# Optimization experiments

Hardware: AMD Instinct MI355X
Metric: run time of the kernel (lower is better)

The kernel has to match this reference:

```python
import jax, jax.numpy as jnp
import numpy as np

N_CELL, N_TISSUE, H, NH = 200000, 2000, 256, 8
HD = H // NH
SCALE = HD ** -0.5
EPS = 1e-5


def _layernorm(x, g, b):
    m = jnp.mean(x, axis=-1, keepdims=True)
    v = jnp.mean((x - m) ** 2, axis=-1, keepdims=True)
    return (x - m) / jnp.sqrt(v + EPS) * g + b


def setup_inputs() -> dict:
    key = jax.random.key(0)
    ks = jax.random.split(key, 12)
    s = 0.02

    def lin(k):
        k1, k2 = jax.random.split(k)
        return (jax.random.normal(k1, (H, H), jnp.float32) * s,
                jax.random.normal(k2, (H,), jnp.float32) * s)

    Wq_bu, bq_bu = lin(ks[0])
    Wk_bu, bk_bu = lin(ks[1])
    Wv_bu, bv_bu = lin(ks[2])
    Wo_bu, bo_bu = lin(ks[3])
    Wv_td, bv_td = lin(ks[4])
    Wo_td, bo_td = lin(ks[5])
    return dict(
        cell_features=jax.random.normal(ks[6], (N_CELL, H), jnp.float32),
        tissue_features=jax.random.normal(ks[7], (N_TISSUE, H), jnp.float32),
        cluster_labels=jax.random.randint(ks[8], (N_CELL,), 0, N_TISSUE, dtype=jnp.int32),
        tissue_batch=jnp.zeros((N_TISSUE,), jnp.int32),
        Wq_bu=Wq_bu, bq_bu=bq_bu, Wk_bu=Wk_bu, bk_bu=bk_bu,
        Wv_bu=Wv_bu, bv_bu=bv_bu, Wo_bu=Wo_bu, bo_bu=bo_bu,
        Wv_td=Wv_td, bv_td=bv_td, Wo_td=Wo_td, bo_td=bo_td,
        ln_cell_g=jnp.ones((H,), jnp.float32), ln_cell_b=jnp.zeros((H,), jnp.float32),
        ln_tissue_g=jnp.ones((H,), jnp.float32), ln_tissue_b=jnp.zeros((H,), jnp.float32),
    )


def reference(cell_features, tissue_features, cluster_labels, tissue_batch,
              Wq_bu, bq_bu, Wk_bu, bk_bu, Wv_bu, bv_bu, Wo_bu, bo_bu,
              Wv_td, bv_td, Wo_td, bo_td,
              ln_cell_g, ln_cell_b, ln_tissue_g, ln_tissue_b):
    Nc = cell_features.shape[0]
    Nt = tissue_features.shape[0]

    # ---- bottom-up: each tissue node (1 query) attends over its cells (segment attention) ----
    Q = (tissue_features @ Wq_bu + bq_bu).reshape(Nt, NH, HD)   # [Nt, h, d]
    K = (cell_features @ Wk_bu + bk_bu).reshape(Nc, NH, HD)     # [Nc, h, d]
    V = (cell_features @ Wv_bu + bv_bu).reshape(Nc, NH, HD)     # [Nc, h, d]

    # per-cell score against its own cluster's tissue query
    scores = jnp.einsum('nhd,nhd->nh', K, Q[cluster_labels]) * SCALE  # [Nc, h]
    smax = jax.lax.stop_gradient(
        jax.ops.segment_max(scores, cluster_labels, num_segments=Nt))  # [Nt, h]
    ex = jnp.exp(scores - smax[cluster_labels])
    denom = jax.ops.segment_sum(ex, cluster_labels, num_segments=Nt)   # [Nt, h]
    w = ex / denom[cluster_labels]                                     # [Nc, h]
    attended = jax.ops.segment_sum(w[..., None] * V, cluster_labels,
                                   num_segments=Nt)                    # [Nt, h, d]
    attended = attended.reshape(Nt, H) @ Wo_bu + bo_bu

    counts = jax.ops.segment_sum(jnp.ones((Nc,), cell_features.dtype),
                                 cluster_labels, num_segments=Nt)
    tissue_updated = jnp.where(counts[:, None] > 0, attended, tissue_features)

    # ---- top-down: each cell attends to its single tissue token ----
    # softmax over a single key is identically 1, so q/k projections cancel:
    # attended_cell = out_proj(v_proj(tissue_updated[cluster]))
    td_per_tissue = (tissue_updated @ Wv_td + bv_td) @ Wo_td + bo_td   # [Nt, H]
    cell_updated = td_per_tissue[cluster_labels]                       # [Nc, H]

    cell_out = _layernorm(cell_features + cell_updated, ln_cell_g, ln_cell_b)
    tissue_out = _layernorm(tissue_features + tissue_updated, ln_tissue_g, ln_tissue_b)
    return (cell_out, tissue_out)
```

## Files before the change

### kernel.cpp

```cpp
#include <hip/hip_runtime.h>
#include <math.h>

#define NC 200000
#define NT 2000
#define HH 256
#define NH_ 8
#define SCALE 0.17677669529663687f
#define EPS 1e-5f
#define SLICE 128
#define PSLICES (NT + NC / SLICE + 1)
#define PSTRIDE 2056


__global__ void k_hist(const int* __restrict__ labels, int* __restrict__ counts) {
  int i = blockIdx.x * 256 + threadIdx.x;
  if (i < NC) atomicAdd(&counts[labels[i]], 1);
}

__global__ void k_scan(const int* __restrict__ counts, int* __restrict__ offsets,
                       int* __restrict__ soff) {
  int tid = threadIdx.x;
  int base = tid * 32;
  int la[32], lb[32];
  int sa = 0, sb = 0;
  #pragma unroll
  for (int k = 0; k < 32; k++) {
    int idx = base + k;
    int v = (idx < NT) ? counts[idx] : 0;
    la[k] = sa; lb[k] = sb;
    sa += v; sb += (v + SLICE - 1) / SLICE;
  }
  int ia_ = sa, ib_ = sb;
  #pragma unroll
  for (int d = 1; d < 64; d <<= 1) {
    int oa = __shfl_up(ia_, d, 64);
    int ob = __shfl_up(ib_, d, 64);
    if (tid >= d) { ia_ += oa; ib_ += ob; }
  }
  int ea = ia_ - sa, eb = ib_ - sb;
  #pragma unroll
  for (int k = 0; k < 32; k++) {
    int idx = base + k;
    if (idx < NT) { offsets[idx] = ea + la[k]; soff[idx] = eb + lb[k]; }
  }
  if (tid == 63) { offsets[NT] = ia_; soff[NT] = ib_; }
}

__global__ void k_slicemap(const int* __restrict__ soff, int* __restrict__ slice_t) {
  int t = blockIdx.x * 256 + threadIdx.x;
  if (t < NT) {
    int s0 = soff[t], s1 = soff[t + 1];
    for (int s = s0; s < s1; s++) slice_t[s] = t;
  }
}

__global__ void k_scatter(const int* __restrict__ labels, const int* __restrict__ offsets,
                          int* __restrict__ cursor, int* __restrict__ cindex) {
  int i = blockIdx.x * 256 + threadIdx.x;
  if (i < NC) {
    int c = labels[i];
    int pos = offsets[c] + atomicAdd(&cursor[c], 1);
    cindex[pos] = i;
  }
}


__global__ __launch_bounds__(256) void k_gemm_bias(
    const float* __restrict__ A, const float* __restrict__ W,
    const float* __restrict__ bias, float* __restrict__ C, int M)
{
  __shared__ float Al[16][33];
  __shared__ float Wl[32][HH];
  int tid = threadIdx.x;
  int r0 = blockIdx.x * 16;
  float acc[16];
  #pragma unroll
  for (int r = 0; r < 16; r++) acc[r] = 0.f;
  for (int k0 = 0; k0 < HH; k0 += 32) {
    for (int e = tid; e < 16 * 32; e += 256) {
      int r = e >> 5, k = e & 31;
      int row = r0 + r;
      Al[r][k] = (row < M) ? A[(size_t)row * HH + k0 + k] : 0.f;
    }
    for (int e = tid; e < 32 * HH; e += 256) {
      int k = e >> 8, j = e & 255;
      Wl[k][j] = W[(size_t)(k0 + k) * HH + j];
    }
    __syncthreads();
    for (int k = 0; k < 32; k++) {
      float w = Wl[k][tid];
      #pragma unroll
      for (int r = 0; r < 16; r++) acc[r] += Al[r][k] * w;
    }
    __syncthreads();
  }
  float bj = bias[tid];
  #pragma unroll
  for (int r = 0; r < 16; r++) {
    int row = r0 + r;
    if (row < M) C[(size_t)row * HH + tid] = acc[r] + bj;
  }
}


__global__ __launch_bounds__(256) void k_qproj(
    const float* __restrict__ Q, const float* __restrict__ Wk, float* __restrict__ Qproj)
{
  __shared__ float Al[64][33];
  __shared__ float Bl[32][257];
  int h = blockIdx.x & 7, tb = blockIdx.x >> 3;
  int t0 = tb * 64;
  int tid = threadIdx.x;
  for (int e = tid; e < 64 * 32; e += 256) {
    int r = e >> 5, d = e & 31;
    int t = t0 + r;
    Al[r][d] = (t < NT) ? Q[(size_t)t * HH + h * 32 + d] * SCALE : 0.f;
  }
  for (int e = tid; e < 256 * 32; e += 256) {
    int j = e >> 5, d = e & 31;
    Bl[d][j] = Wk[(size_t)j * HH + h * 32 + d];
  }
  __syncthreads();
  float acc[64];
  #pragma unroll
  for (int r = 0; r < 64; r++) acc[r] = 0.f;
  for (int d = 0; d < 32; d++) {
    float b = Bl[d][tid];
    #pragma unroll
    for (int r = 0; r < 64; r++) acc[r] += Al[r][d] * b;
  }
  for (int r = 0; r < 64; r++) {
    int t = t0 + r;
    if (t < NT) Qproj[((size_t)t * NH_ + h) * HH + tid] = acc[r];
  }
}

__global__ void k_bkq(const float* __restrict__ Q, const float* __restrict__ bk,
                      float* __restrict__ bkq) {
  int g = blockIdx.x * 256 + threadIdx.x;
  if (g < NT * NH_) {
    int t = g >> 3, h = g & 7;
    float s = 0.f;
    #pragma unroll
    for (int d = 0; d < 32; d++) s += bk[h * 32 + d] * Q[(size_t)t * HH + h * 32 + d];
    bkq[g] = s * SCALE;
  }
}


__global__ __launch_bounds__(256) void k_cellslice(
    const float* __restrict__ cell, const int* __restrict__ cindex,
    const int* __restrict__ offsets, const int* __restrict__ soff,
    const int* __restrict__ slice_t,
    const float* __restrict__ Qproj, const float* __restrict__ bkq,
    float* __restrict__ Pbuf)
{
  __shared__ float qp[NH_][HH];
  __shared__ float e_lds[SLICE][NH_];
  __shared__ float cwlds[NH_][HH];
  __shared__ float red[4][NH_];

  int s = blockIdx.x;
  if (s >= soff[NT]) return;
  int t = slice_t[s];
  int l = s - soff[t];
  int c0 = offsets[t] + l * SLICE;
  int c1 = min(c0 + SLICE, offsets[t + 1]);
  int nc = c1 - c0;

  int tid = threadIdx.x;
  int w = tid >> 6, lane = tid & 63, slot = lane >> 3, g = lane & 7;

  for (int e = tid; e < NH_ * HH / 4; e += 256)
    ((float4*)qp)[e] = ((const float4*)(Qproj + (size_t)t * NH_ * HH))[e];
  float bq[NH_];
  #pragma unroll
  for (int h = 0; h < NH_; h++) bq[h] = bkq[t * NH_ + h];
  __syncthreads();

  int nsweep = (nc + 15) >> 4;
  for (int j = w; j < nsweep; j += 4) {
    int bb = c0 + j * 16;
    int ia = bb + slot, ib = bb + 8 + slot;
    int na = cindex[min(ia, c1 - 1)];
    int nb = cindex[min(ib, c1 - 1)];
    float4 xa[8], xb[8];
    #pragma unroll
    for (int k = 0; k < 8; k++)
      xa[k] = *reinterpret_cast<const float4*>(&cell[(size_t)na * HH + g * 4 + 32 * k]);
    #pragma unroll
    for (int k = 0; k < 8; k++)
      xb[k] = *reinterpret_cast<const float4*>(&cell[(size_t)nb * HH + g * 4 + 32 * k]);

    float pa[NH_], pb[NH_];
    #pragma unroll
    for (int h = 0; h < NH_; h++) { pa[h] = 0.f; pb[h] = 0.f; }
    #pragma unroll
    for (int h = 0; h < NH_; h++) {
      #pragma unroll
      for (int k = 0; k < 8; k++) {
        float4 q = *reinterpret_cast<const float4*>(&qp[h][g * 4 + 32 * k]);
        pa[h] += xa[k].x * q.x + xa[k].y * q.y + xa[k].z * q.z + xa[k].w * q.w;
        pb[h] += xb[k].x * q.x + xb[k].y * q.y + xb[k].z * q.z + xb[k].w * q.w;
      }
    }
    #pragma unroll
    for (int d = 1; d < 8; d <<= 1) {
      #pragma unroll
      for (int h = 0; h < NH_; h++) {
        pa[h] += __shfl_xor(pa[h], d, 64);
        pb[h] += __shfl_xor(pb[h], d, 64);
      }
    }
    float ea[NH_], eb[NH_];
    #pragma unroll
    for (int h = 0; h < NH_; h++) {
      ea[h] = __expf(pa[h] + bq[h]);
      eb[h] = __expf(pb[h] + bq[h]);
    }
    if (g == 0) {
      if (ia < c1) {
        *reinterpret_cast<float4*>(&e_lds[ia - c0][0]) = make_float4(ea[0], ea[1], ea[2], ea[3]);
        *reinterpret_cast<float4*>(&e_lds[ia - c0][4]) = make_float4(ea[4], ea[5], ea[6], ea[7]);
      }
      if (ib < c1) {
        *reinterpret_cast<float4*>(&e_lds[ib - c0][0]) = make_float4(eb[0], eb[1], eb[2], eb[3]);
        *reinterpret_cast<float4*>(&e_lds[ib - c0][4]) = make_float4(eb[4], eb[5], eb[6], eb[7]);
      }
    }
  }
  __syncthreads();

  float cw[NH_][4];
  float dsum[NH_];
  #pragma unroll
  for (int h = 0; h < NH_; h++) {
    cw[h][0] = cw[h][1] = cw[h][2] = cw[h][3] = 0.f;
    dsum[h] = 0.f;
  }
  for (int i = w; i < nc; i += 4) {
    int n = cindex[c0 + i];
    float4 x = *reinterpret_cast<const float4*>(&cell[(size_t)n * HH + lane * 4]);
    float4 e0 = *reinterpret_cast<float4*>(&e_lds[i][0]);
    float4 e1 = *reinterpret_cast<float4*>(&e_lds[i][4]);
    cw[0][0] += e0.x * x.x; cw[0][1] += e0.x * x.y; cw[0][2] += e0.x * x.z; cw[0][3] += e0.x * x.w;
    cw[1][0] += e0.y * x.x; cw[1][1] += e0.y * x.y; cw[1][2] += e0.y * x.z; cw[1][3] += e0.y * x.w;
    cw[2][0] += e0.z * x.x; cw[2][1] += e0.z * x.y; cw[2][2] += e0.z * x.z; cw[2][3] += e0.z * x.w;
    cw[3][0] += e0.w * x.x; cw[3][1] += e0.w * x.y; cw[3][2] += e0.w * x.z; cw[3][3] += e0.w * x.w;
    cw[4][0] += e1.x * x.x; cw[4][1] += e1.x * x.y; cw[4][2] += e1.x * x.z; cw[4][3] += e1.x * x.w;
    cw[5][0] += e1.y * x.x; cw[5][1] += e1.y * x.y; cw[5][2] += e1.y * x.z; cw[5][3] += e1.y * x.w;
    cw[6][0] += e1.z * x.x; cw[6][1] += e1.z * x.y; cw[6][2] += e1.z * x.z; cw[6][3] += e1.z * x.w;
    cw[7][0] += e1.w * x.x; cw[7][1] += e1.w * x.y; cw[7][2] += e1.w * x.z; cw[7][3] += e1.w * x.w;
    dsum[0] += e0.x; dsum[1] += e0.y; dsum[2] += e0.z; dsum[3] += e0.w;
    dsum[4] += e1.x; dsum[5] += e1.y; dsum[6] += e1.z; dsum[7] += e1.w;
  }
  if (lane == 0) {
    #pragma unroll
    for (int h = 0; h < NH_; h++) red[w][h] = dsum[h];
  }
  if (w == 0) {
    #pragma unroll
    for (int h = 0; h < NH_; h++)
      *reinterpret_cast<float4*>(&cwlds[h][lane * 4]) =
          make_float4(cw[h][0], cw[h][1], cw[h][2], cw[h][3]);
  }
  __syncthreads();
  #pragma unroll
  for (int ww = 1; ww < 4; ww++) {
    if (w == ww) {
      #pragma unroll
      for (int h = 0; h < NH_; h++) {
        float4 c = *reinterpret_cast<float4*>(&cwlds[h][lane * 4]);
        c.x += cw[h][0]; c.y += cw[h][1]; c.z += cw[h][2]; c.w += cw[h][3];
        *reinterpret_cast<float4*>(&cwlds[h][lane * 4]) = c;
      }
    }
    __syncthreads();
  }

  float* pb = Pbuf + (size_t)s * PSTRIDE;
  #pragma unroll
  for (int h = 0; h < NH_; h++) pb[h * HH + tid] = cwlds[h][tid];
  if (tid < NH_) pb[2048 + tid] = red[0][tid] + red[1][tid] + red[2][tid] + red[3][tid];
}


__global__ __launch_bounds__(256) void k_reduce(
    const float* __restrict__ Pbuf, const int* __restrict__ soff, float* __restrict__ Cwn)
{
  int t = blockIdx.x;
  int s0 = soff[t], ns = soff[t + 1] - s0;
  int tid = threadIdx.x;
  #pragma unroll
  for (int r = 0; r < 2; r++) {
    int c4 = tid + r * 256;
    int h = c4 >> 6;
    float4 acc = make_float4(0.f, 0.f, 0.f, 0.f);
    float d = 0.f;
    for (int q = 0; q < ns; q++) {
      const float* p = Pbuf + (size_t)(s0 + q) * PSTRIDE;
      float4 v = *reinterpret_cast<const float4*>(&p[c4 * 4]);
      acc.x += v.x; acc.y += v.y; acc.z += v.z; acc.w += v.w;
      d += p[2048 + h];
    }
    float inv = (ns > 0) ? 1.f / d : 0.f;
    float4 o = make_float4(acc.x * inv, acc.y * inv, acc.z * inv, acc.w * inv);
    *reinterpret_cast<float4*>(&Cwn[(size_t)t * 2048 + c4 * 4]) = o;
  }
}


#define TCH 8

__global__ __launch_bounds__(256) void k_tissuechain(
    const float* __restrict__ tissue, const int* __restrict__ counts,
    const float* __restrict__ Cwn,
    const float* __restrict__ Wv, const float* __restrict__ bv,
    const float* __restrict__ Wo, const float* __restrict__ bo,
    const float* __restrict__ Wvtd, const float* __restrict__ bvtd,
    const float* __restrict__ Wotd, const float* __restrict__ botd,
    const float* __restrict__ lng, const float* __restrict__ lnb,
    float* __restrict__ td, float* __restrict__ out_tissue)
{
  __shared__ float s_cwn[TCH][NH_ * HH];
  __shared__ float s_a[TCH][HH];
  __shared__ float s_tu[TCH][HH];
  __shared__ float s_tmp[TCH][HH];
  __shared__ float s_red[2][4];
  int t0 = blockIdx.x * TCH;
  int j = threadIdx.x;
  int h = j >> 5;

  for (int e = j; e < TCH * NH_ * HH; e += 256)
    ((float*)s_cwn)[e] = Cwn[(size_t)t0 * NH_ * HH + e];
  __syncthreads();

  float acc[TCH];
  #pragma unroll
  for (int t = 0; t < TCH; t++) acc[t] = 0.f;
  for (int k = 0; k < HH; k++) {
    float w = Wv[(size_t)k * HH + j];
    #pragma unroll
    for (int t = 0; t < TCH; t++) acc[t] += s_cwn[t][h * HH + k] * w;
  }
  {
    float bj = bv[j];
    #pragma unroll
    for (int t = 0; t < TCH; t++) s_a[t][j] = acc[t] + bj;
  }
  __syncthreads();

  #pragma unroll
  for (int t = 0; t < TCH; t++) acc[t] = 0.f;
  for (int k = 0; k < HH; k++) {
    float w = Wo[(size_t)k * HH + j];
    #pragma unroll
    for (int t = 0; t < TCH; t++) acc[t] += s_a[t][k] * w;
  }
  {
    float bj = bo[j];
    #pragma unroll
    for (int t = 0; t < TCH; t++) {
      int tt = t0 + t;
      s_tu[t][j] = (counts[tt] > 0) ? (acc[t] + bj) : tissue[(size_t)tt * HH + j];
    }
  }
  __syncthreads();

  #pragma unroll
  for (int t = 0; t < TCH; t++) acc[t] = 0.f;
  for (int k = 0; k < HH; k++) {
    float w = Wvtd[(size_t)k * HH + j];
    #pragma unroll
    for (int t = 0; t < TCH; t++) acc[t] += s_tu[t][k] * w;
  }
  {
    float bj = bvtd[j];
    #pragma unroll
    for (int t = 0; t < TCH; t++) s_tmp[t][j] = acc[t] + bj;
  }
  __syncthreads();

  #pragma unroll
  for (int t = 0; t < TCH; t++) acc[t] = 0.f;
  for (int k = 0; k < HH; k++) {
    float w = Wotd[(size_t)k * HH + j];
    #pragma unroll
    for (int t = 0; t < TCH; t++) acc[t] += s_tmp[t][k] * w;
  }
  {
    float bj = botd[j];
    #pragma unroll
    for (int t = 0; t < TCH; t++) td[(size_t)(t0 + t) * HH + j] = acc[t] + bj;
  }

  float gj = lng[j], bj2 = lnb[j];
  for (int t = 0; t < TCH; t++) {
    float y = tissue[(size_t)(t0 + t) * HH + j] + s_tu[t][j];
    float s1 = y, s2 = y * y;
    #pragma unroll
    for (int d = 1; d < 64; d <<= 1) { s1 += __shfl_xor(s1, d, 64); s2 += __shfl_xor(s2, d, 64); }
    int wv_ = j >> 6, ln_ = j & 63;
    __syncthreads();
    if (ln_ == 0) { s_red[0][wv_] = s1; s_red[1][wv_] = s2; }
    __syncthreads();
    s1 = s_red[0][0] + s_red[0][1] + s_red[0][2] + s_red[0][3];
    s2 = s_red[1][0] + s_red[1][1] + s_red[1][2] + s_red[1][3];
    float mean = s1 * (1.f / 256.f);
    float var = s2 * (1.f / 256.f) - mean * mean;
    float inv = rsqrtf(var + EPS);
    out_tissue[(size_t)(t0 + t) * HH + j] = (y - mean) * inv * gj + bj2;
  }
}


__global__ __launch_bounds__(256) void k_cellout(
    const float* __restrict__ cell, const float* __restrict__ td,
    const int* __restrict__ labels,
    const float* __restrict__ lng, const float* __restrict__ lnb,
    float* __restrict__ out)
{
  int row = blockIdx.x * 4 + (threadIdx.x >> 6);
  if (row >= NC) return;
  int lane = threadIdx.x & 63;
  int c = labels[row];
  float4 x = *reinterpret_cast<const float4*>(&cell[(size_t)row * HH + lane * 4]);
  float4 u = *reinterpret_cast<const float4*>(&td[(size_t)c * HH + lane * 4]);
  float y0 = x.x + u.x, y1 = x.y + u.y, y2 = x.z + u.z, y3 = x.w + u.w;
  float s1 = y0 + y1 + y2 + y3;
  float s2 = y0 * y0 + y1 * y1 + y2 * y2 + y3 * y3;
  #pragma unroll
  for (int d = 1; d < 64; d <<= 1) { s1 += __shfl_xor(s1, d, 64); s2 += __shfl_xor(s2, d, 64); }
  float mean = s1 * (1.f / 256.f);
  float var = s2 * (1.f / 256.f) - mean * mean;
  float inv = rsqrtf(var + EPS);
  float4 g = *reinterpret_cast<const float4*>(&lng[lane * 4]);
  float4 b = *reinterpret_cast<const float4*>(&lnb[lane * 4]);
  float4 o;
  o.x = (y0 - mean) * inv * g.x + b.x;
  o.y = (y1 - mean) * inv * g.y + b.y;
  o.z = (y2 - mean) * inv * g.z + b.z;
  o.w = (y3 - mean) * inv * g.w + b.w;
  *reinterpret_cast<float4*>(&out[(size_t)row * HH + lane * 4]) = o;
}


extern "C" void kernel_launch(void* const* d_in, const int* in_sizes, int n_in,
                              void* d_out, int out_size, void* d_ws, size_t ws_size,
                              hipStream_t stream) {
  const float* cell   = (const float*)d_in[0];
  const float* tissue = (const float*)d_in[1];
  const int*   labels = (const int*)d_in[2];
  const float* Wq = (const float*)d_in[4];  const float* bq = (const float*)d_in[5];
  const float* Wk = (const float*)d_in[6];  const float* bk = (const float*)d_in[7];
  const float* Wv = (const float*)d_in[8];  const float* bv = (const float*)d_in[9];
  const float* Wo = (const float*)d_in[10]; const float* bo = (const float*)d_in[11];
  const float* Wvtd = (const float*)d_in[12]; const float* bvtd = (const float*)d_in[13];
  const float* Wotd = (const float*)d_in[14]; const float* botd = (const float*)d_in[15];
  const float* lncg = (const float*)d_in[16]; const float* lncb = (const float*)d_in[17];
  const float* lntg = (const float*)d_in[18]; const float* lntb = (const float*)d_in[19];
  float* out_cell   = (float*)d_out;
  float* out_tissue = (float*)d_out + (size_t)NC * HH;

  char* w = (char*)d_ws;
  auto take = [&](size_t bytes) { void* p = (void*)w; w += (bytes + 255) & ~(size_t)255; return p; };
  int*   counts  = (int*)take((size_t)NT * 4);
  int*   cursor  = (int*)take((size_t)NT * 4);
  int*   offsets = (int*)take((size_t)(NT + 1) * 4);
  int*   soff    = (int*)take((size_t)(NT + 1) * 4);
  int*   slice_t = (int*)take((size_t)PSLICES * 4);
  int*   cindex  = (int*)take((size_t)NC * 4);
  float* Q       = (float*)take((size_t)NT * HH * 4);
  float* Qproj   = (float*)take((size_t)NT * NH_ * HH * 4);
  float* bkq     = (float*)take((size_t)NT * NH_ * 4);
  float* Cwn     = (float*)take((size_t)NT * NH_ * HH * 4);
  float* td      = (float*)take((size_t)NT * HH * 4);
  float* Pbuf    = (float*)take((size_t)PSLICES * PSTRIDE * 4);

  hipMemsetAsync(counts, 0, 16384, stream);

  const int CB = (NC + 255) / 256;
  k_hist<<<CB, 256, 0, stream>>>(labels, counts);
  k_scan<<<1, 64, 0, stream>>>(counts, offsets, soff);
  k_slicemap<<<(NT + 255) / 256, 256, 0, stream>>>(soff, slice_t);
  k_scatter<<<CB, 256, 0, stream>>>(labels, offsets, cursor, cindex);

  k_gemm_bias<<<(NT + 15) / 16, 256, 0, stream>>>(tissue, Wq, bq, Q, NT);
  k_qproj<<<8 * ((NT + 63) / 64), 256, 0, stream>>>(Q, Wk, Qproj);
  k_bkq<<<(NT * NH_ + 255) / 256, 256, 0, stream>>>(Q, bk, bkq);

  k_cellslice<<<PSLICES, 256, 0, stream>>>(cell, cindex, offsets, soff, slice_t,
                                           Qproj, bkq, Pbuf);
  k_reduce<<<NT, 256, 0, stream>>>(Pbuf, soff, Cwn);

  k_tissuechain<<<NT / TCH, 256, 0, stream>>>(tissue, counts, Cwn,
      Wv, bv, Wo, bo, Wvtd, bvtd, Wotd, botd, lntg, lntb, td, out_tissue);

  k_cellout<<<NC / 4, 256, 0, stream>>>(cell, td, labels, lncg, lncb, out_cell);
}
```

Before: 489.2 us.

## Fuse small prep kernels, fold partial reduce into tissue chain, batch cell-slice loads

Three small kernels are folded into their neighbours, which removes three launches and the Cwn intermediate buffer. The slice-map fill moves into the scan kernel, the bias-query dot product moves into the Q-projection kernel, and the per-slice partial reduction moves into the tissue-chain kernel. In the cell-slice kernel, cell indices are staged in LDS and the weighted-sum loop processes four cells per iteration to expose more memory-level parallelism. The exp is computed only on the writing lane, and a launch_bounds occupancy hint is added. Risks: the single-wave scan now does serial slice writes, and the tissue chain re-reads soff for every element of its gather loop.

After: 666.1 us. +36.2%, slower.

```diff
diff --git a/kernel.cpp b/kernel.cpp
--- a/kernel.cpp
+++ b/kernel.cpp
@@ -18,17 +18,18 @@
 }
 
 __global__ void k_scan(const int* __restrict__ counts, int* __restrict__ offsets,
-                       int* __restrict__ soff) {
+                       int* __restrict__ soff, int* __restrict__ slice_t) {
   int tid = threadIdx.x;
   int base = tid * 32;
-  int la[32], lb[32];
+  int la[32], lb[32], scnt[32];
   int sa = 0, sb = 0;
   #pragma unroll
   for (int k = 0; k < 32; k++) {
     int idx = base + k;
     int v = (idx < NT) ? counts[idx] : 0;
     la[k] = sa; lb[k] = sb;
-    sa += v; sb += (v + SLICE - 1) / SLICE;
+    scnt[k] = (v + SLICE - 1) / SLICE;
+    sa += v; sb += scnt[k];
   }
   int ia_ = sa, ib_ = sb;
   #pragma unroll
@@ -41,17 +42,14 @@
   #pragma unroll
   for (int k = 0; k < 32; k++) {
     int idx = base + k;
-    if (idx < NT) { offsets[idx] = ea + la[k]; soff[idx] = eb + lb[k]; }
+    if (idx < NT) {
+      offsets[idx] = ea + la[k];
+      soff[idx] = eb + lb[k];
+      int st = eb + lb[k];
+      for (int s2 = 0; s2 < scnt[k]; s2++) slice_t[st + s2] = idx;
+    }
   }
   if (tid == 63) { offsets[NT] = ia_; soff[NT] = ib_; }
-}
-
-__global__ void k_slicemap(const int* __restrict__ soff, int* __restrict__ slice_t) {
-  int t = blockIdx.x * 256 + threadIdx.x;
-  if (t < NT) {
-    int s0 = soff[t], s1 = soff[t + 1];
-    for (int s = s0; s < s1; s++) slice_t[s] = t;
-  }
 }
 
 __global__ void k_scatter(const int* __restrict__ labels, const int* __restrict__ offsets,
@@ -104,7 +102,9 @@
 
 
 __global__ __launch_bounds__(256) void k_qproj(
-    const float* __restrict__ Q, const float* __restrict__ Wk, float* __restrict__ Qproj)
+    const float* __restrict__ Q, const float* __restrict__ Wk,
+    const float* __restrict__ bk, float* __restrict__ Qproj,
+    float* __restrict__ bkq)
 {
   __shared__ float Al[64][33];
   __shared__ float Bl[32][257];
@@ -133,22 +133,19 @@
     int t = t0 + r;
     if (t < NT) Qproj[((size_t)t * NH_ + h) * HH + tid] = acc[r];
   }
-}
-
-__global__ void k_bkq(const float* __restrict__ Q, const float* __restrict__ bk,
-                      float* __restrict__ bkq) {
-  int g = blockIdx.x * 256 + threadIdx.x;
-  if (g < NT * NH_) {
-    int t = g >> 3, h = g & 7;
-    float s = 0.f;
-    #pragma unroll
-    for (int d = 0; d < 32; d++) s += bk[h * 32 + d] * Q[(size_t)t * HH + h * 32 + d];
-    bkq[g] = s * SCALE;
-  }
-}
-
-
-__global__ __launch_bounds__(256) void k_cellslice(
+  if (tid < 64) {
+    int t = t0 + tid;
+    if (t < NT) {
+      float s = 0.f;
+      #pragma unroll
+      for (int d = 0; d < 32; d++) s += Al[tid][d] * bk[h * 32 + d];
+      bkq[t * NH_ + h] = s;
+    }
+  }
+}
+
+
+__global__ __launch_bounds__(256, 4) void k_cellslice(
     const float* __restrict__ cell, const int* __restrict__ cindex,
     const int* __restrict__ offsets, const int* __restrict__ soff,
     const int* __restrict__ slice_t,
@@ -157,6 +154,7 @@
 {
   __shared__ float qp[NH_][HH];
   __shared__ float e_lds[SLICE][NH_];
+  __shared__ int   cidx[SLICE];
   __shared__ float cwlds[NH_][HH];
   __shared__ float red[4][NH_];
 
@@ -167,23 +165,24 @@
   int c0 = offsets[t] + l * SLICE;
   int c1 = min(c0 + SLICE, offsets[t + 1]);
   int nc = c1 - c0;
+  int ncp = (nc + 15) & ~15;
 
   int tid = threadIdx.x;
   int w = tid >> 6, lane = tid & 63, slot = lane >> 3, g = lane & 7;
 
   for (int e = tid; e < NH_ * HH / 4; e += 256)
     ((float4*)qp)[e] = ((const float4*)(Qproj + (size_t)t * NH_ * HH))[e];
+  if (tid < SLICE) cidx[tid] = cindex[min(c0 + tid, c1 - 1)];
+  for (int e = tid; e < SLICE * NH_; e += 256) ((float*)e_lds)[e] = 0.f;
   float bq[NH_];
   #pragma unroll
   for (int h = 0; h < NH_; h++) bq[h] = bkq[t * NH_ + h];
   __syncthreads();
 
-  int nsweep = (nc + 15) >> 4;
+  int nsweep = ncp >> 4;
   for (int j = w; j < nsweep; j += 4) {
-    int bb = c0 + j * 16;
-    int ia = bb + slot, ib = bb + 8 + slot;
-    int na = cindex[min(ia, c1 - 1)];
-    int nb = cindex[min(ib, c1 - 1)];
+    int ia = j * 16 + slot, ib = ia + 8;
+    int na = cidx[ia], nb = cidx[ib];
     float4 xa[8], xb[8];
     #pragma unroll
     for (int k = 0; k < 8; k++)
@@ -212,20 +211,20 @@
         pb[h] += __shfl_xor(pb[h], d, 64);
       }
     }
-    float ea[NH_], eb[NH_];
-    #pragma unroll
-    for (int h = 0; h < NH_; h++) {
-      ea[h] = __expf(pa[h] + bq[h]);
-      eb[h] = __expf(pb[h] + bq[h]);
-    }
     if (g == 0) {
-      if (ia < c1) {
-        *reinterpret_cast<float4*>(&e_lds[ia - c0][0]) = make_float4(ea[0], ea[1], ea[2], ea[3]);
-        *reinterpret_cast<float4*>(&e_lds[ia - c0][4]) = make_float4(ea[4], ea[5], ea[6], ea[7]);
+      if (ia < nc) {
+        float ea[NH_];
+        #pragma unroll
+        for (int h = 0; h < NH_; h++) ea[h] = __expf(pa[h] + bq[h]);
+        *reinterpret_cast<float4*>(&e_lds[ia][0]) = make_float4(ea[0], ea[1], ea[2], ea[3]);
+        *reinterpret_cast<float4*>(&e_lds[ia][4]) = make_float4(ea[4], ea[5], ea[6], ea[7]);
       }
-      if (ib < c1) {
-        *reinterpret_cast<float4*>(&e_lds[ib - c0][0]) = make_float4(eb[0], eb[1], eb[2], eb[3]);
-        *reinterpret_cast<float4*>(&e_lds[ib - c0][4]) = make_float4(eb[4], eb[5], eb[6], eb[7]);
+      if (ib < nc) {
+        float eb[NH_];
+        #pragma unroll
+        for (int h = 0; h < NH_; h++) eb[h] = __expf(pb[h] + bq[h]);
+        *reinterpret_cast<float4*>(&e_lds[ib][0]) = make_float4(eb[0], eb[1], eb[2], eb[3]);
+        *reinterpret_cast<float4*>(&e_lds[ib][4]) = make_float4(eb[4], eb[5], eb[6], eb[7]);
       }
     }
   }
@@ -238,21 +237,30 @@
     cw[h][0] = cw[h][1] = cw[h][2] = cw[h][3] = 0.f;
     dsum[h] = 0.f;
   }
-  for (int i = w; i < nc; i += 4) {
-    int n = cindex[c0 + i];
-    float4 x = *reinterpret_cast<const float4*>(&cell[(size_t)n * HH + lane * 4]);
-    float4 e0 = *reinterpret_cast<float4*>(&e_lds[i][0]);
-    float4 e1 = *reinterpret_cast<float4*>(&e_lds[i][4]);
-    cw[0][0] += e0.x * x.x; cw[0][1] += e0.x * x.y; cw[0][2] += e0.x * x.z; cw[0][3] += e0.x * x.w;
-    cw[1][0] += e0.y * x.x; cw[1][1] += e0.y * x.y; cw[1][2] += e0.y * x.z; cw[1][3] += e0.y * x.w;
-    cw[2][0] += e0.z * x.x; cw[2][1] += e0.z * x.y; cw[2][2] += e0.z * x.z; cw[2][3] += e0.z * x.w;
-    cw[3][0] += e0.w * x.x; cw[3][1] += e0.w * x.y; cw[3][2] += e0.w * x.z; cw[3][3] += e0.w * x.w;
-    cw[4][0] += e1.x * x.x; cw[4][1] += e1.x * x.y; cw[4][2] += e1.x * x.z; cw[4][3] += e1.x * x.w;
-    cw[5][0] += e1.y * x.x; cw[5][1] += e1.y * x.y; cw[5][2] += e1.y * x.z; cw[5][3] += e1.y * x.w;
-    cw[6][0] += e1.z * x.x; cw[6][1] += e1.z * x.y; cw[6][2] += e1.z * x.z; cw[6][3] += e1.z * x.w;
-    cw[7][0] += e1.w * x.x; cw[7][1] += e1.w * x.y; cw[7][2] += e1.w * x.z; cw[7][3] += e1.w * x.w;
-    dsum[0] += e0.x; dsum[1] += e0.y; dsum[2] += e0.z; dsum[3] += e0.w;
-    dsum[4] += e1.x; dsum[5] += e1.y; dsum[6] += e1.z; dsum[7] += e1.w;
+  for (int i = w * 4; i < ncp; i += 16) {
+    int nn[4];
+    #pragma unroll
+    for (int c = 0; c < 4; c++) nn[c] = cidx[i + c];
+    float4 xx[4];
+    #pragma unroll
+    for (int c = 0; c < 4; c++)
+      xx[c] = *reinterpret_cast<const float4*>(&cell[(size_t)nn[c] * HH + lane * 4]);
+    #pragma unroll
+    for (int c = 0; c < 4; c++) {
+      float4 e0 = *reinterpret_cast<float4*>(&e_lds[i + c][0]);
+      float4 e1 = *reinterpret_cast<float4*>(&e_lds[i + c][4]);
+      float4 x = xx[c];
+      cw[0][0] += e0.x * x.x; cw[0][1] += e0.x * x.y; cw[0][2] += e0.x * x.z; cw[0][3] += e0.x * x.w;
+      cw[1][0] += e0.y * x.x; cw[1][1] += e0.y * x.y; cw[1][2] += e0.y * x.z; cw[1][3] += e0.y * x.w;
+      cw[2][0] += e0.z * x.x; cw[2][1] += e0.z * x.y; cw[2][2] += e0.z * x.z; cw[2][3] += e0.z * x.w;
+      cw[3][0] += e0.w * x.x; cw[3][1] += e0.w * x.y; cw[3][2] += e0.w * x.z; cw[3][3] += e0.w * x.w;
+      cw[4][0] += e1.x * x.x; cw[4][1] += e1.x * x.y; cw[4][2] += e1.x * x.z; cw[4][3] += e1.x * x.w;
+      cw[5][0] += e1.y * x.x; cw[5][1] += e1.y * x.y; cw[5][2] += e1.y * x.z; cw[5][3] += e1.y * x.w;
+      cw[6][0] += e1.z * x.x; cw[6][1] += e1.z * x.y; cw[6][2] += e1.z * x.z; cw[6][3] += e1.z * x.w;
+      cw[7][0] += e1.w * x.x; cw[7][1] += e1.w * x.y; cw[7][2] += e1.w * x.z; cw[7][3] += e1.w * x.w;
+      dsum[0] += e0.x; dsum[1] += e0.y; dsum[2] += e0.z; dsum[3] += e0.w;
+      dsum[4] += e1.x; dsum[5] += e1.y; dsum[6] += e1.z; dsum[7] += e1.w;
+    }
   }
   if (lane == 0) {
     #pragma unroll
@@ -285,36 +293,11 @@
 }
 
 
-__global__ __launch_bounds__(256) void k_reduce(
-    const float* __restrict__ Pbuf, const int* __restrict__ soff, float* __restrict__ Cwn)
-{
-  int t = blockIdx.x;
-  int s0 = soff[t], ns = soff[t + 1] - s0;
-  int tid = threadIdx.x;
-  #pragma unroll
-  for (int r = 0; r < 2; r++) {
-    int c4 = tid + r * 256;
-    int h = c4 >> 6;
-    float4 acc = make_float4(0.f, 0.f, 0.f, 0.f);
-    float d = 0.f;
-    for (int q = 0; q < ns; q++) {
-      const float* p = Pbuf + (size_t)(s0 + q) * PSTRIDE;
-      float4 v = *reinterpret_cast<const float4*>(&p[c4 * 4]);
-      acc.x += v.x; acc.y += v.y; acc.z += v.z; acc.w += v.w;
-      d += p[2048 + h];
-    }
-    float inv = (ns > 0) ? 1.f / d : 0.f;
-    float4 o = make_float4(acc.x * inv, acc.y * inv, acc.z * inv, acc.w * inv);
-    *reinterpret_cast<float4*>(&Cwn[(size_t)t * 2048 + c4 * 4]) = o;
-  }
-}
-
-
 #define TCH 8
 
 __global__ __launch_bounds__(256) void k_tissuechain(
     const float* __restrict__ tissue, const int* __restrict__ counts,
-    const float* __restrict__ Cwn,
+    const float* __restrict__ Pbuf, const int* __restrict__ soff,
     const float* __restrict__ Wv, const float* __restrict__ bv,
     const float* __restrict__ Wo, const float* __restrict__ bo,
     const float* __restrict__ Wvtd, const float* __restrict__ bvtd,
@@ -327,12 +310,27 @@
   __shared__ float s_tu[TCH][HH];
   __shared__ float s_tmp[TCH][HH];
   __shared__ float s_red[2][4];
+  __shared__ float s_dinv[TCH][NH_];
   int t0 = blockIdx.x * TCH;
   int j = threadIdx.x;
   int h = j >> 5;
 
-  for (int e = j; e < TCH * NH_ * HH; e += 256)
-    ((float*)s_cwn)[e] = Cwn[(size_t)t0 * NH_ * HH + e];
+  if (j < TCH * NH_) {
+    int t = j >> 3, hh = j & 7;
+    int s0 = soff[t0 + t], s1 = soff[t0 + t + 1];
+    float d = 0.f;
+    for (int q = s0; q < s1; q++) d += Pbuf[(size_t)q * PSTRIDE + 2048 + hh];
+    s_dinv[t][hh] = (s1 > s0) ? 1.f / d : 0.f;
+  }
+  __syncthreads();
+
+  for (int e = j; e < TCH * NH_ * HH; e += 256) {
+    int t = e >> 11, c = e & 2047, hh = c >> 8;
+    int s0 = soff[t0 + t], s1 = soff[t0 + t + 1];
+    float a = 0.f;
+    for (int q = s0; q < s1; q++) a += Pbuf[(size_t)q * PSTRIDE + c];
+    s_cwn[t][c] = a * s_dinv[t][hh];
+  }
   __syncthreads();
 
   float acc[TCH];
@@ -473,7 +471,6 @@
   float* Q       = (float*)take((size_t)NT * HH * 4);
   float* Qproj   = (float*)take((size_t)NT * NH_ * HH * 4);
   float* bkq     = (float*)take((size_t)NT * NH_ * 4);
-  float* Cwn     = (float*)take((size_t)NT * NH_ * HH * 4);
   float* td      = (float*)take((size_t)NT * HH * 4);
   float* Pbuf    = (float*)take((size_t)PSLICES * PSTRIDE * 4);
 
@@ -481,19 +478,16 @@
 
   const int CB = (NC + 255) / 256;
   k_hist<<<CB, 256, 0, stream>>>(labels, counts);
-  k_scan<<<1, 64, 0, stream>>>(counts, offsets, soff);
-  k_slicemap<<<(NT + 255) / 256, 256, 0, stream>>>(soff, slice_t);
+  k_scan<<<1, 64, 0, stream>>>(counts, offsets, soff, slice_t);
   k_scatter<<<CB, 256, 0, stream>>>(labels, offsets, cursor, cindex);
 
   k_gemm_bias<<<(NT + 15) / 16, 256, 0, stream>>>(tissue, Wq, bq, Q, NT);
-  k_qproj<<<8 * ((NT + 63) / 64), 256, 0, stream>>>(Q, Wk, Qproj);
-  k_bkq<<<(NT * NH_ + 255) / 256, 256, 0, stream>>>(Q, bk, bkq);
+  k_qproj<<<8 * ((NT + 63) / 64), 256, 0, stream>>>(Q, Wk, bk, Qproj, bkq);
 
   k_cellslice<<<PSLICES, 256, 0, stream>>>(cell, cindex, offsets, soff, slice_t,
                                            Qproj, bkq, Pbuf);
-  k_reduce<<<NT, 256, 0, stream>>>(Pbuf, soff, Cwn);
-
-  k_tissuechain<<<NT / TCH, 256, 0, stream>>>(tissue, counts, Cwn,
+
+  k_tissuechain<<<NT / TCH, 256, 0, stream>>>(tissue, counts, Pbuf, soff,
       Wv, bv, Wo, bo, Wvtd, bvtd, Wotd, botd, lntg, lntb, td, out_tissue);
 
   k_cellout<<<NC / 4, 256, 0, stream>>>(cell, td, labels, lncg, lncb, out_cell);
```
